# Optimization experiments

Measured on AMD Instinct MI355X. Metric: run time of the kernel, lower is better.

Reference implementation:

```python
import jax, jax.numpy as jnp
import numpy as np

NEG_INF = -1e9  # module uses -1e9 negativeInfinity constant
BS, DA, SL, H = 16, 512, 1024, 8


def setup_inputs() -> dict:
    key = jax.random.key(0)
    ks = jax.random.split(key, 8)
    return {
        "q":    jax.random.normal(ks[0], (BS, DA, SL), dtype=jnp.float32),
        "k_in": jax.random.normal(ks[1], (BS, DA, SL), dtype=jnp.float32),
        "v_in": jax.random.normal(ks[2], (BS, DA, SL), dtype=jnp.float32),
        "k_w":  jax.random.normal(ks[3], (DA, DA), dtype=jnp.float32) * 0.05,
        "k_b":  jax.random.normal(ks[4], (DA,), dtype=jnp.float32) * 0.05,
        "v_w":  jax.random.normal(ks[5], (DA, DA), dtype=jnp.float32) * 0.05,
        "v_b":  jax.random.normal(ks[6], (DA,), dtype=jnp.float32) * 0.05,
        "gbn_gamma": jnp.ones((H,), dtype=jnp.float32),
        "gbn_bias":  jnp.zeros((H,), dtype=jnp.float32),
        "gbn_m":     jnp.zeros((H,), dtype=jnp.float32),
        "gbn_s":     jnp.ones((H,), dtype=jnp.float32),
        "mask": jax.random.randint(ks[7], (BS, 1, 1, SL), 0, 2, dtype=jnp.int32),
    }


def reference(q, k_in, v_in, k_w, k_b, v_w, v_b, gbn_gamma, gbn_bias, gbn_m, gbn_s, mask):
    bs, da, qsl = q.shape
    h = gbn_gamma.shape[0]
    dh = da // h
    sl = k_in.shape[2]
    mask_b = mask.astype(bool)                 # [bs,1,1,sl] True = masked

    # 1x1 conv1d projections == per-position matmul over channels
    k = jnp.einsum('ok,bks->bos', k_w, k_in) + k_b[None, :, None]   # [bs,da,sl]
    v = jnp.einsum('ov,bvs->bos', v_w, v_in) + v_b[None, :, None]   # [bs,dva,sl]
    dva = v.shape[1]
    dvh = dva // h

    qh = q.reshape(bs, h, dh, qsl).transpose(0, 1, 3, 2)   # [bs,h,qsl,dh]
    kh = k.reshape(bs, h, dh, sl)                          # [bs,h,dh,sl]
    vh = v.reshape(bs, h, dvh, sl).transpose(0, 1, 3, 2)   # [bs,h,sl,dvh]

    scores = jnp.einsum('bhqd,bhds->bhqs', qh, kh)         # [bs,h,qsl,sl]

    # GhostBatchNorm1d(features=h) in eval mode: per-head affine normalization
    scores = (scores - gbn_m[None, :, None, None]) / gbn_s[None, :, None, None]
    scores = scores * gbn_gamma[None, :, None, None] + gbn_bias[None, :, None, None]

    mask_k = mask_b                           # [bs,1,1,sl]  mask key positions (selfAttention fill)
    mask_q = jnp.swapaxes(mask_b, 2, 3)       # [bs,1,sl,1]  mask query rows (transposed fill)
    scores = jnp.where(mask_k, NEG_INF, scores)
    scores = jnp.where(mask_q, NEG_INF, scores)

    w = jax.nn.softmax(scores, axis=-1)
    w = jnp.where(mask_q, 0.0, w)             # v_weights.masked_fill(mask, 0)

    out = jnp.einsum('bhqs,bhsd->bhqd', w, vh)             # [bs,h,qsl,dvh]
    out = out.transpose(0, 1, 3, 2).reshape(bs, dva, qsl)  # back to channels-first
    return out
```

## Files before the change

kernel.cpp:

```cpp
#include <hip/hip_runtime.h>

typedef _Float16 f16;
typedef _Float16 h8_t __attribute__((ext_vector_type(8)));
typedef _Float16 h4_t __attribute__((ext_vector_type(4)));
typedef float f32x4 __attribute__((ext_vector_type(4)));
typedef float f32x16 __attribute__((ext_vector_type(16)));

#define BS 16
#define DA 512
#define SL 1024
#define NH 8
#define DH 64

__device__ __forceinline__ void gload_lds16(const void* g, void* l) {
  __builtin_amdgcn_global_load_lds((const __attribute__((address_space(1))) void*)g,
                                   (__attribute__((address_space(3))) void*)l, 16, 0, 0);
}

__global__ __launch_bounds__(256) void prep_kernel(
    const float* __restrict__ k_in, const float* __restrict__ v_in,
    const float* __restrict__ k_w, const float* __restrict__ v_w,
    f16* __restrict__ Kt, f16* __restrict__ Vt,
    f16* __restrict__ kwh, f16* __restrict__ vwh) {
  const int blk = blockIdx.x;
  const int t = threadIdx.x;
  if (blk < 2048) {
    const int which = blk >> 10;
    const int r = blk & 1023;
    const int b = r >> 6;
    const int c0 = ((r >> 3) & 7) * 64;
    const int s0 = (r & 7) * 128;
    const float* src = which ? v_in : k_in;
    f16* dst = which ? Vt : Kt;
    __shared__ __align__(16) float Xf32[64 * 132];
#pragma unroll
    for (int p = 0; p < 8; ++p) {
      const int idx = p * 256 + t;
      const int cc = idx >> 5, s4 = (idx & 31) * 4;
      const float4 v = *(const float4*)&src[((size_t)b * DA + c0 + cc) * SL + s0 + s4];
      *(float4*)&Xf32[cc * 132 + s4] = v;
    }
    __syncthreads();
    const int srow = t >> 1, cb = (t & 1) * 32;
#pragma unroll
    for (int g = 0; g < 4; ++g) {
      h8_t h;
#pragma unroll
      for (int u = 0; u < 8; ++u) h[u] = (f16)Xf32[(cb + g * 8 + u) * 132 + srow];
      *(h8_t*)&dst[((size_t)b * SL + s0 + srow) * DA + c0 + cb + g * 8] = h;
    }
  } else {
    const int r = blk - 2048;
    const int wsel = r >> 5;
    const float* src = wsel ? v_w : k_w;
    f16* dst = wsel ? vwh : kwh;
    const int base = (r & 31) * 8192;
#pragma unroll
    for (int p = 0; p < 4; ++p) {
      const int i = base + p * 2048 + t * 8;
      const float4 a = *(const float4*)&src[i];
      const float4 c = *(const float4*)&src[i + 4];
      h8_t h;
      h[0] = (f16)a.x; h[1] = (f16)a.y; h[2] = (f16)a.z; h[3] = (f16)a.w;
      h[4] = (f16)c.x; h[5] = (f16)c.y; h[6] = (f16)c.z; h[7] = (f16)c.w;
      *(h8_t*)&dst[i] = h;
    }
  }
}

__global__ __launch_bounds__(256, 4) void proj_gemm_all(
    const f16* __restrict__ kwh, const f16* __restrict__ vwh,
    const f16* __restrict__ Kt, const f16* __restrict__ Vt,
    const float* __restrict__ k_b, const float* __restrict__ v_b,
    f16* __restrict__ kp, f16* __restrict__ vp) {
  __shared__ __align__(16) f16 LD[2][8192];
  const int mode = blockIdx.z;
  const int b = blockIdx.y;
  const int tx = blockIdx.x;
  const int m0 = (mode ? (tx >> 2) : (tx & 3)) * 128;
  const int n0 = (mode ? (tx & 3) : (tx >> 2)) * 128;
  const int t = threadIdx.x;
  const int lane = t & 63, w = t >> 6, lr = lane & 15, lq = lane >> 4;
  const int wm = (w >> 1) * 64, wn = (w & 1) * 64;

  const f16* Arow = (mode ? Vt + (size_t)b * SL * DA : kwh) + (size_t)m0 * DA;
  const f16* Brow = (mode ? vwh : Kt + (size_t)b * SL * DA) + (size_t)n0 * DA;

  const int rr = t >> 2;
  const int c8 = (t & 3) * 8;
  const int lo8 = t * 8;

  const f16* ga0 = Arow + (size_t)rr * DA + c8;
  const f16* ga1 = Arow + (size_t)(64 + rr) * DA + c8;
  const f16* gb0 = Brow + (size_t)rr * DA + c8;
  const f16* gb1 = Brow + (size_t)(64 + rr) * DA + c8;

  f32x4 acc[4][4] = {};

  gload_lds16(ga0, &LD[0][0] + lo8);
  gload_lds16(ga1, &LD[0][2048] + lo8);
  gload_lds16(gb0, &LD[0][4096] + lo8);
  gload_lds16(gb1, &LD[0][6144] + lo8);
  ga0 += 32; ga1 += 32; gb0 += 32; gb1 += 32;
  __syncthreads();

  for (int kt = 0; kt < 16; ++kt) {
    const int cur = kt & 1;
    if (kt < 15) {
      f16* nb = &LD[cur ^ 1][0];
      gload_lds16(ga0, nb + lo8);
      gload_lds16(ga1, nb + 2048 + lo8);
      gload_lds16(gb0, nb + 4096 + lo8);
      gload_lds16(gb1, nb + 6144 + lo8);
      ga0 += 32; ga1 += 32; gb0 += 32; gb1 += 32;
    }
    const f16* Al = &LD[cur][0];
    const f16* Bl = &LD[cur][4096];
    h8_t af[4], bf[4];
#pragma unroll
    for (int i = 0; i < 4; ++i) af[i] = *(const h8_t*)&Al[(wm + i * 16 + lr) * 32 + lq * 8];
#pragma unroll
    for (int j = 0; j < 4; ++j) bf[j] = *(const h8_t*)&Bl[(wn + j * 16 + lr) * 32 + lq * 8];
    __builtin_amdgcn_s_setprio(1);
#pragma unroll
    for (int i = 0; i < 4; ++i)
#pragma unroll
      for (int j = 0; j < 4; ++j)
        acc[i][j] = __builtin_amdgcn_mfma_f32_16x16x32_f16(af[i], bf[j], acc[i][j], 0, 0, 0);
    __builtin_amdgcn_s_setprio(0);
    __syncthreads();
  }

#pragma unroll
  for (int i = 0; i < 4; ++i) {
    const int gmb = m0 + wm + i * 16 + lq * 4;
    float bm[4] = {0.f, 0.f, 0.f, 0.f};
    if (mode == 0) {
      const float4 b4 = *(const float4*)&k_b[gmb];
      bm[0] = b4.x; bm[1] = b4.y; bm[2] = b4.z; bm[3] = b4.w;
    }
#pragma unroll
    for (int j = 0; j < 4; ++j) {
      const int gn = n0 + wn + j * 16 + lr;
      const float bn = mode ? v_b[gn] : 0.f;
      h4_t hv;
#pragma unroll
      for (int r = 0; r < 4; ++r) {
        const float val = acc[i][j][r] + (mode == 0 ? bm[r] : bn);
        hv[r] = (f16)val;
      }
      f16* dst = mode ? &vp[((size_t)b * DA + gn) * SL + gmb]
                      : &kp[((size_t)b * SL + gn) * DA + gmb];
      *(h4_t*)dst = hv;
    }
  }
}

template <int MODE>
__global__ __launch_bounds__(256) void fused_proj(const float* __restrict__ Wg,
                                                  const float* __restrict__ Xin,
                                                  const float* __restrict__ bias,
                                                  f16* __restrict__ outg) {
  constexpr int MT = MODE ? SL : DA;
  constexpr int NT = MODE ? DA : SL;
  __shared__ f16 Wl[128 * 40];
  __shared__ f16 Xl[128 * 40];
  __shared__ float Xf32[32 * 132];
  const int b = blockIdx.z;
  const int m0 = blockIdx.x * 128;
  const int n0 = blockIdx.y * 128;
  const int o_base = MODE ? n0 : m0;
  const int s_base = MODE ? m0 : n0;
  const int t = threadIdx.x;
  const int w = t >> 6, lane = t & 63, lr = lane & 15, lq = lane >> 4;
  const int wm = (w >> 1) * 64, wn = (w & 1) * 64;

  f32x4 acc[4][4] = {};

  for (int kt = 0; kt < 16; ++kt) {
    const int c0 = kt * 32;
    __syncthreads();
#pragma unroll
    for (int p = 0; p < 4; ++p) {
      const int idx = p * 256 + t;
      const int row = idx >> 3, cq = (idx & 7) * 4;
      const float4 v = *(const float4*)&Wg[(size_t)(o_base + row) * DA + c0 + cq];
      h4_t hv;
      hv[0] = (f16)v.x; hv[1] = (f16)v.y; hv[2] = (f16)v.z; hv[3] = (f16)v.w;
      *(h4_t*)&Wl[row * 40 + cq] = hv;
    }
#pragma unroll
    for (int p = 0; p < 4; ++p) {
      const int idx = p * 256 + t;
      const int cc = idx >> 5, s4 = (idx & 31) * 4;
      const float4 v = *(const float4*)&Xin[((size_t)b * DA + c0 + cc) * SL + s_base + s4];
      *(float4*)&Xf32[cc * 132 + s4] = v;
    }
    __syncthreads();
    {
      const int srow = t >> 1, cb = (t & 1) * 16;
      h8_t lo, hi;
#pragma unroll
      for (int u = 0; u < 8; ++u) lo[u] = (f16)Xf32[(cb + u) * 132 + srow];
#pragma unroll
      for (int u = 0; u < 8; ++u) hi[u] = (f16)Xf32[(cb + 8 + u) * 132 + srow];
      *(h8_t*)&Xl[srow * 40 + cb] = lo;
      *(h8_t*)&Xl[srow * 40 + cb + 8] = hi;
    }
    __syncthreads();
    const f16* Alp = MODE ? Xl : Wl;
    const f16* Blp = MODE ? Wl : Xl;
    h8_t af[4], bf[4];
#pragma unroll
    for (int i = 0; i < 4; ++i) af[i] = *(const h8_t*)&Alp[(wm + i * 16 + lr) * 40 + lq * 8];
#pragma unroll
    for (int j = 0; j < 4; ++j) bf[j] = *(const h8_t*)&Blp[(wn + j * 16 + lr) * 40 + lq * 8];
#pragma unroll
    for (int i = 0; i < 4; ++i)
#pragma unroll
      for (int j = 0; j < 4; ++j)
        acc[i][j] = __builtin_amdgcn_mfma_f32_16x16x32_f16(af[i], bf[j], acc[i][j], 0, 0, 0);
  }

#pragma unroll
  for (int i = 0; i < 4; ++i) {
    const int gmb = m0 + wm + i * 16 + lq * 4;
    float bm[4] = {0.f, 0.f, 0.f, 0.f};
    if (MODE == 0) {
      const float4 b4 = *(const float4*)&bias[gmb];
      bm[0] = b4.x; bm[1] = b4.y; bm[2] = b4.z; bm[3] = b4.w;
    }
#pragma unroll
    for (int j = 0; j < 4; ++j) {
      const int gn = n0 + wn + j * 16 + lr;
      const float bn = (MODE == 1) ? bias[gn] : 0.f;
      h4_t hv;
#pragma unroll
      for (int r = 0; r < 4; ++r) {
        const float val = acc[i][j][r] + (MODE == 0 ? bm[r] : bn);
        hv[r] = (f16)val;
      }
      *(h4_t*)&outg[((size_t)b * NT + gn) * MT + gmb] = hv;
    }
  }
}

__global__ __launch_bounds__(256, 4) void attn_kernel(
    const float* __restrict__ qg, const f16* __restrict__ kp, const f16* __restrict__ vp,
    const float* __restrict__ gamma, const float* __restrict__ gbns,
    const int* __restrict__ maskg, float* __restrict__ outg) {
  __shared__ __align__(16) char smem[36864];
  f16* KV = (f16*)smem;
  float* Osh = (float*)smem;

  const int bh = blockIdx.x, b = bh >> 3, h = bh & 7;
  const int i0 = blockIdx.y * 128;
  const int t = threadIdx.x, w = t >> 6, lane = t & 63;
  const int l5 = lane & 31, hf = lane >> 5;
  const float scale = gamma[h] / gbns[h] * 1.44269504088896f;
  const int iw = i0 + w * 32 + l5;

  h8_t qf[4];
#pragma unroll
  for (int ks = 0; ks < 4; ++ks) {
    h8_t v;
#pragma unroll
    for (int u = 0; u < 8; ++u) {
      const int d = ks * 16 + hf * 8 + u;
      v[u] = (f16)(qg[((size_t)b * DA + h * DH + d) * SL + iw] * scale);
    }
    qf[ks] = v;
  }

  const int srow = t >> 3;
  const int c8 = (t & 7) * 8;

  uint4 rk[2], rv[2];
#pragma unroll
  for (int p = 0; p < 2; ++p) {
    const int row = p * 32 + srow;
    rk[p] = *(const uint4*)&kp[((size_t)b * SL + row) * DA + h * DH + c8];
    rv[p] = *(const uint4*)&vp[((size_t)b * DA + h * DH + row) * SL + c8];
  }
  {
    f16* K0 = KV;
    f16* V0 = KV + 4608;
#pragma unroll
    for (int p = 0; p < 2; ++p) {
      const int row = p * 32 + srow;
      const int rowp = (row & ~12) | ((row & 4) << 1) | ((row & 8) >> 1);
      *(uint4*)&K0[rowp * 72 + c8] = rk[p];
      *(uint4*)&V0[row * 72 + c8] = rv[p];
    }
  }
  __syncthreads();

  float m_i = -3e38f, l_i = 0.f;
  f32x16 acc[2] = {};

  for (int jt = 0; jt < 16; ++jt) {
    const int j0 = jt * 64;
    const f16* Kc = KV + (jt & 1) * 9216;
    const f16* Vc = Kc + 4608;

    if (jt < 15) {
      const int jn = j0 + 64;
#pragma unroll
      for (int p = 0; p < 2; ++p) {
        const int row = p * 32 + srow;
        rk[p] = *(const uint4*)&kp[((size_t)b * SL + jn + row) * DA + h * DH + c8];
        rv[p] = *(const uint4*)&vp[((size_t)b * DA + h * DH + row) * SL + jn + c8];
      }
    }
    int4 mq[2][4];
#pragma unroll
    for (int mj = 0; mj < 2; ++mj)
#pragma unroll
      for (int q = 0; q < 4; ++q)
        mq[mj][q] = *(const int4*)&maskg[b * SL + j0 + mj * 32 + (q >> 1) * 16 + hf * 8 + (q & 1) * 4];

    f32x16 sa[2] = {};
    __builtin_amdgcn_s_setprio(1);
#pragma unroll
    for (int ks = 0; ks < 4; ++ks)
#pragma unroll
      for (int mj = 0; mj < 2; ++mj) {
        const h8_t kf = *(const h8_t*)&Kc[(mj * 32 + l5) * 72 + ks * 16 + hf * 8];
        sa[mj] = __builtin_amdgcn_mfma_f32_32x32x16_f16(kf, qf[ks], sa[mj], 0, 0, 0);
      }
    __builtin_amdgcn_s_setprio(0);

#pragma unroll
    for (int mj = 0; mj < 2; ++mj)
#pragma unroll
      for (int q = 0; q < 4; ++q) {
        const int4 m4 = mq[mj][q];
        if (m4.x) sa[mj][q * 4 + 0] = -1e9f;
        if (m4.y) sa[mj][q * 4 + 1] = -1e9f;
        if (m4.z) sa[mj][q * 4 + 2] = -1e9f;
        if (m4.w) sa[mj][q * 4 + 3] = -1e9f;
      }

    float mx;
    {
      float a[8];
#pragma unroll
      for (int u = 0; u < 8; ++u)
        a[u] = fmaxf(fmaxf(sa[0][u], sa[0][u + 8]), fmaxf(sa[1][u], sa[1][u + 8]));
      const float b0 = fmaxf(a[0], a[1]), b1 = fmaxf(a[2], a[3]);
      const float b2 = fmaxf(a[4], a[5]), b3 = fmaxf(a[6], a[7]);
      mx = fmaxf(fmaxf(b0, b1), fmaxf(b2, b3));
      mx = fmaxf(mx, __shfl_xor(mx, 32));
    }
    if (!__all(mx - m_i <= 8.0f)) {
      const float mn = fmaxf(m_i, mx);
      const float alpha = __builtin_amdgcn_exp2f(m_i - mn);
      m_i = mn;
      l_i *= alpha;
#pragma unroll
      for (int nd = 0; nd < 2; ++nd)
#pragma unroll
        for (int e = 0; e < 16; ++e) acc[nd][e] *= alpha;
    }
    {
      float r0 = 0.f, r1 = 0.f, r2 = 0.f, r3 = 0.f;
#pragma unroll
      for (int mj = 0; mj < 2; ++mj)
#pragma unroll
        for (int e = 0; e < 16; e += 4) {
          const float p0 = __builtin_amdgcn_exp2f(sa[mj][e + 0] - m_i);
          const float p1 = __builtin_amdgcn_exp2f(sa[mj][e + 1] - m_i);
          const float p2 = __builtin_amdgcn_exp2f(sa[mj][e + 2] - m_i);
          const float p3 = __builtin_amdgcn_exp2f(sa[mj][e + 3] - m_i);
          sa[mj][e + 0] = p0; sa[mj][e + 1] = p1;
          sa[mj][e + 2] = p2; sa[mj][e + 3] = p3;
          r0 += p0; r1 += p1; r2 += p2; r3 += p3;
        }
      float rs = (r0 + r1) + (r2 + r3);
      rs += __shfl_xor(rs, 32);
      l_i += rs;
    }

    __builtin_amdgcn_s_setprio(1);
#pragma unroll
    for (int jk = 0; jk < 4; ++jk) {
      const int mj = jk >> 1, g = jk & 1;
      h8_t pk;
#pragma unroll
      for (int u = 0; u < 8; ++u) pk[u] = (f16)sa[mj][g * 8 + u];
#pragma unroll
      for (int nd = 0; nd < 2; ++nd) {
        const h8_t vf = *(const h8_t*)&Vc[(nd * 32 + l5) * 72 + jk * 16 + hf * 8];
        acc[nd] = __builtin_amdgcn_mfma_f32_32x32x16_f16(vf, pk, acc[nd], 0, 0, 0);
      }
    }
    __builtin_amdgcn_s_setprio(0);

    if (jt < 15) {
      f16* Kn = KV + ((jt + 1) & 1) * 9216;
      f16* Vn = Kn + 4608;
#pragma unroll
      for (int p = 0; p < 2; ++p) {
        const int row = p * 32 + srow;
        const int rowp = (row & ~12) | ((row & 4) << 1) | ((row & 8) >> 1);
        *(uint4*)&Kn[rowp * 72 + c8] = rk[p];
        *(uint4*)&Vn[row * 72 + c8] = rv[p];
      }
      __syncthreads();
    }
  }

  const int mo = maskg[b * SL + iw];
  const float fac = mo ? 0.f : 1.f / l_i;
  __syncthreads();

#pragma unroll
  for (int nd = 0; nd < 2; ++nd) {
#pragma unroll
    for (int e = 0; e < 16; ++e) {
      const int dl = (e & 3) + 8 * (e >> 2) + 4 * hf;
      Osh[dl * 128 + w * 32 + l5] = acc[nd][e] * fac;
    }
    __syncthreads();
#pragma unroll
    for (int pass = 0; pass < 4; ++pass) {
      const int row = pass * 8 + (t >> 5);
      const int i4 = (t & 31) * 4;
      const float4 o = *(const float4*)&Osh[row * 128 + i4];
      *(float4*)&outg[((size_t)b * DA + h * DH + nd * 32 + row) * SL + i0 + i4] = o;
    }
    __syncthreads();
  }
}

extern "C" void kernel_launch(void* const* d_in, const int* in_sizes, int n_in,
                              void* d_out, int out_size, void* d_ws, size_t ws_size,
                              hipStream_t stream) {
  const float* q     = (const float*)d_in[0];
  const float* k_in  = (const float*)d_in[1];
  const float* v_in  = (const float*)d_in[2];
  const float* k_w   = (const float*)d_in[3];
  const float* k_b   = (const float*)d_in[4];
  const float* v_w   = (const float*)d_in[5];
  const float* v_b   = (const float*)d_in[6];
  const float* gamma = (const float*)d_in[7];
  const float* gbns  = (const float*)d_in[10];
  const int*   mask  = (const int*)d_in[11];
  float* out = (float*)d_out;

  const size_t NEL = (size_t)BS * SL * DA;
  f16* kpw = (f16*)d_ws;
  f16* vpw = kpw + NEL;

  const size_t need = NEL * 2 * 4 + (size_t)DA * DA * 2 * 2;
  if (ws_size >= need) {
    f16* Kt  = vpw + NEL;
    f16* Vt  = Kt + NEL;
    f16* kwh = Vt + NEL;
    f16* vwh = kwh + (size_t)DA * DA;
    prep_kernel<<<dim3(2112), 256, 0, stream>>>(k_in, v_in, k_w, v_w, Kt, Vt, kwh, vwh);
    proj_gemm_all<<<dim3(32, BS, 2), 256, 0, stream>>>(kwh, vwh, Kt, Vt, k_b, v_b, kpw, vpw);
  } else {
    fused_proj<0><<<dim3(4, 8, BS), 256, 0, stream>>>(k_w, k_in, k_b, kpw);
    fused_proj<1><<<dim3(8, 4, BS), 256, 0, stream>>>(v_w, v_in, v_b, vpw);
  }
  attn_kernel<<<dim3(BS * NH, SL / 128), 256, 0, stream>>>(q, kpw, vpw, gamma, gbns, mask, out);
}
```

Measured before the change: 263.9 us.

## Enlarge attention query tile to 256 rows and precompute mask bias in LDS

Result: faster. 236.7 us (-10.3%).

```diff
diff --git a/kernel.cpp b/kernel.cpp
--- a/kernel.cpp
+++ b/kernel.cpp
@@ -245,16 +245,17 @@
   }
 }
 
-__global__ __launch_bounds__(256, 4) void attn_kernel(
+__global__ __launch_bounds__(512, 4) void attn_kernel(
     const float* __restrict__ qg, const f16* __restrict__ kp, const f16* __restrict__ vp,
     const float* __restrict__ gamma, const float* __restrict__ gbns,
     const int* __restrict__ maskg, float* __restrict__ outg) {
-  __shared__ __align__(16) char smem[36864];
+  __shared__ __align__(16) char smem[36864 + 4096];
   f16* KV = (f16*)smem;
   float* Osh = (float*)smem;
+  float* biasf = (float*)(smem + 36864);
 
   const int bh = blockIdx.x, b = bh >> 3, h = bh & 7;
-  const int i0 = blockIdx.y * 128;
+  const int i0 = blockIdx.y * 256;
   const int t = threadIdx.x, w = t >> 6, lane = t & 63;
   const int l5 = lane & 31, hf = lane >> 5;
   const float scale = gamma[h] / gbns[h] * 1.44269504088896f;
@@ -272,26 +273,23 @@
     qf[ks] = v;
   }
 
+  {
+    const int2 m2 = *(const int2*)&maskg[b * SL + t * 2];
+    biasf[t * 2 + 0] = m2.x ? -1e9f : 0.f;
+    biasf[t * 2 + 1] = m2.y ? -1e9f : 0.f;
+  }
+
   const int srow = t >> 3;
   const int c8 = (t & 7) * 8;
 
-  uint4 rk[2], rv[2];
-#pragma unroll
-  for (int p = 0; p < 2; ++p) {
-    const int row = p * 32 + srow;
-    rk[p] = *(const uint4*)&kp[((size_t)b * SL + row) * DA + h * DH + c8];
-    rv[p] = *(const uint4*)&vp[((size_t)b * DA + h * DH + row) * SL + c8];
-  }
+  uint4 rk = *(const uint4*)&kp[((size_t)b * SL + srow) * DA + h * DH + c8];
+  uint4 rv = *(const uint4*)&vp[((size_t)b * DA + h * DH + srow) * SL + c8];
   {
     f16* K0 = KV;
     f16* V0 = KV + 4608;
-#pragma unroll
-    for (int p = 0; p < 2; ++p) {
-      const int row = p * 32 + srow;
-      const int rowp = (row & ~12) | ((row & 4) << 1) | ((row & 8) >> 1);
-      *(uint4*)&K0[rowp * 72 + c8] = rk[p];
-      *(uint4*)&V0[row * 72 + c8] = rv[p];
-    }
+    const int rowp = (srow & ~12) | ((srow & 4) << 1) | ((srow & 8) >> 1);
+    *(uint4*)&K0[rowp * 72 + c8] = rk;
+    *(uint4*)&V0[srow * 72 + c8] = rv;
   }
   __syncthreads();
 
@@ -305,19 +303,9 @@
 
     if (jt < 15) {
       const int jn = j0 + 64;
-#pragma unroll
-      for (int p = 0; p < 2; ++p) {
-        const int row = p * 32 + srow;
-        rk[p] = *(const uint4*)&kp[((size_t)b * SL + jn + row) * DA + h * DH + c8];
-        rv[p] = *(const uint4*)&vp[((size_t)b * DA + h * DH + row) * SL + jn + c8];
-      }
-    }
-    int4 mq[2][4];
-#pragma unroll
-    for (int mj = 0; mj < 2; ++mj)
-#pragma unroll
-      for (int q = 0; q < 4; ++q)
-        mq[mj][q] = *(const int4*)&maskg[b * SL + j0 + mj * 32 + (q >> 1) * 16 + hf * 8 + (q & 1) * 4];
+      rk = *(const uint4*)&kp[((size_t)b * SL + jn + srow) * DA + h * DH + c8];
+      rv = *(const uint4*)&vp[((size_t)b * DA + h * DH + srow) * SL + jn + c8];
+    }
 
     f32x16 sa[2] = {};
     __builtin_amdgcn_s_setprio(1);
@@ -333,36 +321,32 @@
 #pragma unroll
     for (int mj = 0; mj < 2; ++mj)
 #pragma unroll
-      for (int q = 0; q < 4; ++q) {
-        const int4 m4 = mq[mj][q];
-        if (m4.x) sa[mj][q * 4 + 0] = -1e9f;
-        if (m4.y) sa[mj][q * 4 + 1] = -1e9f;
-        if (m4.z) sa[mj][q * 4 + 2] = -1e9f;
-        if (m4.w) sa[mj][q * 4 + 3] = -1e9f;
-      }
-
-    float mx;
+      for (int qq = 0; qq < 4; ++qq) {
+        const float4 bq = *(const float4*)&biasf[j0 + mj * 32 + (qq >> 1) * 16 + hf * 8 + (qq & 1) * 4];
+        sa[mj][qq * 4 + 0] += bq.x;
+        sa[mj][qq * 4 + 1] += bq.y;
+        sa[mj][qq * 4 + 2] += bq.z;
+        sa[mj][qq * 4 + 3] += bq.w;
+      }
+
     {
       float a[8];
 #pragma unroll
       for (int u = 0; u < 8; ++u)
         a[u] = fmaxf(fmaxf(sa[0][u], sa[0][u + 8]), fmaxf(sa[1][u], sa[1][u + 8]));
-      const float b0 = fmaxf(a[0], a[1]), b1 = fmaxf(a[2], a[3]);
-      const float b2 = fmaxf(a[4], a[5]), b3 = fmaxf(a[6], a[7]);
-      mx = fmaxf(fmaxf(b0, b1), fmaxf(b2, b3));
+      float mx = fmaxf(fmaxf(fmaxf(a[0], a[1]), fmaxf(a[2], a[3])),
+                       fmaxf(fmaxf(a[4], a[5]), fmaxf(a[6], a[7])));
       mx = fmaxf(mx, __shfl_xor(mx, 32));
-    }
-    if (!__all(mx - m_i <= 8.0f)) {
-      const float mn = fmaxf(m_i, mx);
-      const float alpha = __builtin_amdgcn_exp2f(m_i - mn);
-      m_i = mn;
-      l_i *= alpha;
-#pragma unroll
-      for (int nd = 0; nd < 2; ++nd)
-#pragma unroll
-        for (int e = 0; e < 16; ++e) acc[nd][e] *= alpha;
-    }
-    {
+      if (!__all(mx - m_i <= 8.0f)) {
+        const float mn = fmaxf(m_i, mx);
+        const float alpha = __builtin_amdgcn_exp2f(m_i - mn);
+        m_i = mn;
+        l_i *= alpha;
+#pragma unroll
+        for (int nd = 0; nd < 2; ++nd)
+#pragma unroll
+          for (int e = 0; e < 16; ++e) acc[nd][e] *= alpha;
+      }
       float r0 = 0.f, r1 = 0.f, r2 = 0.f, r3 = 0.f;
 #pragma unroll
       for (int mj = 0; mj < 2; ++mj)
@@ -399,13 +383,9 @@
     if (jt < 15) {
       f16* Kn = KV + ((jt + 1) & 1) * 9216;
       f16* Vn = Kn + 4608;
-#pragma unroll
-      for (int p = 0; p < 2; ++p) {
-        const int row = p * 32 + srow;
-        const int rowp = (row & ~12) | ((row & 4) << 1) | ((row & 8) >> 1);
-        *(uint4*)&Kn[rowp * 72 + c8] = rk[p];
-        *(uint4*)&Vn[row * 72 + c8] = rv[p];
-      }
+      const int rowp = (srow & ~12) | ((srow & 4) << 1) | ((srow & 8) >> 1);
+      *(uint4*)&Kn[rowp * 72 + c8] = rk;
+      *(uint4*)&Vn[srow * 72 + c8] = rv;
       __syncthreads();
     }
   }
@@ -419,14 +399,14 @@
 #pragma unroll
     for (int e = 0; e < 16; ++e) {
       const int dl = (e & 3) + 8 * (e >> 2) + 4 * hf;
-      Osh[dl * 128 + w * 32 + l5] = acc[nd][e] * fac;
+      Osh[dl * 256 + w * 32 + l5] = acc[nd][e] * fac;
     }
     __syncthreads();
 #pragma unroll
     for (int pass = 0; pass < 4; ++pass) {
-      const int row = pass * 8 + (t >> 5);
-      const int i4 = (t & 31) * 4;
-      const float4 o = *(const float4*)&Osh[row * 128 + i4];
+      const int row = pass * 8 + (t >> 6);
+      const int i4 = (t & 63) * 4;
+      const float4 o = *(const float4*)&Osh[row * 256 + i4];
       *(float4*)&outg[((size_t)b * DA + h * DH + nd * 32 + row) * SL + i0 + i4] = o;
     }
     __syncthreads();
@@ -464,5 +444,5 @@
     fused_proj<0><<<dim3(4, 8, BS), 256, 0, stream>>>(k_w, k_in, k_b, kpw);
     fused_proj<1><<<dim3(8, 4, BS), 256, 0, stream>>>(v_w, v_in, v_b, vpw);
   }
-  attn_kernel<<<dim3(BS * NH, SL / 128), 256, 0, stream>>>(q, kpw, vpw, gamma, gbns, mask, out);
-}
+  attn_kernel<<<dim3(BS * NH, SL / 256), 512, 0, stream>>>(q, kpw, vpw, gamma, gbns, mask, out);
+}
```
